# Performance work log

Measured on AMD Instinct MI355X. Metric: run time of the kernel, lower is better.

Reference implementation:

```python
import jax, jax.numpy as jnp
import numpy as np

EPS = 1e-8

def rms_norm(x, scale):
    # norm(2,-1)/sqrt(d); x / (rms + eps) * scale
    d = x.shape[-1]
    norm = jnp.sqrt(jnp.sum(x * x, axis=-1, keepdims=True))
    rms = norm / jnp.sqrt(jnp.asarray(d, x.dtype))
    return scale * (x / (rms + EPS))

def setup_inputs() -> dict:
    key = jax.random.key(0)
    B, N, C, FF = 2, 2048, 1024, 4096
    ks = jax.random.split(key, 12)
    s = 0.02
    return {
        "x":  jax.random.normal(ks[0], (B, N, C), jnp.float32),
        "wq": jax.random.normal(ks[1], (C, C), jnp.float32) * s,
        "bq": jnp.zeros((C,), jnp.float32),
        "wk": jax.random.normal(ks[2], (C, C), jnp.float32) * s,
        "bk": jnp.zeros((C,), jnp.float32),
        "wv": jax.random.normal(ks[3], (C, C), jnp.float32) * s,
        "bv": jnp.zeros((C,), jnp.float32),
        "wo": jax.random.normal(ks[4], (C, C), jnp.float32) * s,
        "bo": jnp.zeros((C,), jnp.float32),
        "scale1": jnp.ones((C,), jnp.float32),
        "scale2": jnp.ones((C,), jnp.float32),
        "w1": jax.random.normal(ks[5], (C, FF), jnp.float32) * s,
        "b1": jnp.zeros((FF,), jnp.float32),
        "w2": jax.random.normal(ks[6], (FF, C), jnp.float32) * s,
        "b2": jnp.zeros((C,), jnp.float32),
    }

def reference(x, wq, bq, wk, bk, wv, bv, wo, bo, scale1, scale2, w1, b1, w2, b2):
    B, N, C = x.shape
    H = 16
    D = C // H

    residual = x
    xn = rms_norm(x, scale1)

    def heads(y):  # [B,N,C] -> [B,H,N,D]
        return y.reshape(B, N, H, D).transpose(0, 2, 1, 3)

    q = heads(xn @ wq + bq)
    k = heads(xn @ wk + bk)
    v = heads(xn @ wv + bv)

    # apply_rotary_pos_emb with cos=sin=1: q' = q - roll(q,1,-1), same for k
    q = q - jnp.roll(q, 1, axis=-1)
    k = k - jnp.roll(k, 1, axis=-1)

    # explicit attention (no causal mask in original)
    scores = jnp.einsum('bhnd,bhmd->bhnm', q, k) / jnp.sqrt(jnp.asarray(D, x.dtype))
    probs = jax.nn.softmax(scores, axis=-1)
    attn = jnp.einsum('bhnm,bhmd->bhnd', probs, v)
    attn = attn.transpose(0, 2, 1, 3).reshape(B, N, C)
    attn = attn @ wo + bo

    x = residual + attn
    residual = x
    xn = rms_norm(x, scale2)
    h = jax.nn.gelu(xn @ w1 + b1, approximate=False)  # torch GELU default = exact
    ffn_out = h @ w2 + b2
    return residual + ffn_out
```

## Files before the change

### kernel.cpp

```cpp
#include <hip/hip_runtime.h>
#include <hip/hip_bf16.h>
#include <math.h>

typedef unsigned short u16;
typedef short s16x8 __attribute__((ext_vector_type(8)));
typedef short s16x4 __attribute__((ext_vector_type(4)));
typedef __bf16 bf16x8v __attribute__((ext_vector_type(8)));
typedef float f32x4 __attribute__((ext_vector_type(4)));
typedef unsigned short u16x4 __attribute__((ext_vector_type(4)));

struct Ptr4 { float* p[4]; };
struct TW6 {
    const float* w[6]; u16* o[6]; int mode[6];
    const float *bq, *bk, *bv; float* bqkv;
};

__device__ __forceinline__ u16 f2b(float f) {
    __hip_bfloat16 h = __float2bfloat16(f);
    return __builtin_bit_cast(u16, h);
}

__device__ __forceinline__ float exp2_fast(float x) {
#if __has_builtin(__builtin_amdgcn_exp2f)
    return __builtin_amdgcn_exp2f(x);
#else
    return exp2f(x);
#endif
}

__device__ __forceinline__ f32x4 mfma16(s16x8 a, s16x8 b, f32x4 c) {
    return __builtin_amdgcn_mfma_f32_16x16x32_bf16(
        __builtin_bit_cast(bf16x8v, a), __builtin_bit_cast(bf16x8v, b), c, 0, 0, 0);
}

__device__ __forceinline__ void gl_lds16(const void* g, void* l) {
    typedef const unsigned int __attribute__((address_space(1))) * gp_t;
    typedef unsigned int __attribute__((address_space(3))) * lp_t;
    __builtin_amdgcn_global_load_lds((gp_t)(unsigned long long)g,
                                     (lp_t)(unsigned int)(unsigned long long)l,
                                     16, 0, 0);
}

__device__ __forceinline__ float gelu_fast(float v) {
    float u = 1.5957691216f * (v + 0.044715f * v * v * v);
    return v / (1.f + __expf(-u));
}

#define QSCALE 0.1803368801111244f

__global__ __launch_bounds__(256) void prep_weights(TW6 io) {
    const int z = blockIdx.z, bx = blockIdx.x, by = blockIdx.y;
    const float* W; u16* Wt; int mode = 0, N_, K_, n0, k0;
    if (z < 4) {
        if (bx >= 32) {
            if (z == 0 && bx < 44 && by == 0) {
                const int i = (bx - 32) * 256 + threadIdx.x;
                const int d = i & 1023;
                const int dp = (d & ~63) | ((d + 63) & 63);
                float v;
                if (i < 1024) v = QSCALE * (io.bq[d] - io.bq[dp]);
                else if (i < 2048) v = io.bk[d] - io.bk[dp];
                else v = io.bv[d];
                io.bqkv[i] = v;
            }
            return;
        }
        W = io.w[z]; Wt = io.o[z]; mode = io.mode[z];
        N_ = 1024; K_ = 1024; n0 = bx * 32; k0 = by * 32;
    } else if (z == 4) {
        W = io.w[4]; Wt = io.o[4]; N_ = 4096; K_ = 1024; n0 = bx * 32; k0 = by * 32;
    } else {
        W = io.w[5]; Wt = io.o[5]; N_ = 1024; K_ = 4096; n0 = by * 32; k0 = bx * 32;
    }
    __shared__ u16 tile[32][33];
    const int tx = threadIdx.x & 31, ty = threadIdx.x >> 5;
    const int n = n0 + tx;
    const int np = (n & ~63) | ((n + 63) & 63);
    const float s = (mode == 1) ? QSCALE : 1.f;
#pragma unroll
    for (int i = 0; i < 32; i += 8) {
        const size_t r = (size_t)(k0 + ty + i) * N_;
        float v = W[r + n];
        if (mode) v = (v - W[r + np]) * s;
        tile[ty + i][tx] = f2b(v);
    }
    __syncthreads();
#pragma unroll
    for (int i = 0; i < 32; i += 8)
        Wt[(size_t)(n0 + ty + i) * K_ + k0 + tx] = tile[tx][ty + i];
}

__global__ __launch_bounds__(256) void transpose_v(const u16* __restrict__ qkv,
                                                   u16* __restrict__ vT) {
    __shared__ u16 tile[32][33];
    const int tx = threadIdx.x & 31, ty = threadIdx.x >> 5;
    const int n0 = blockIdx.x * 32, d0 = blockIdx.y * 32, bh = blockIdx.z;
    const int b = bh >> 4, h = bh & 15;
#pragma unroll
    for (int i = 0; i < 32; i += 8)
        tile[ty + i][tx] =
            qkv[(size_t)(b * 2048 + n0 + ty + i) * 3072 + 2048 + h * 64 + d0 + tx];
    __syncthreads();
#pragma unroll
    for (int i = 0; i < 32; i += 8)
        vT[((size_t)bh * 64 + d0 + ty + i) * 2048 + n0 + tx] = tile[tx][ty + i];
}

__global__ __launch_bounds__(256) void rmsnorm_kernel(const float* __restrict__ x,
                                                      const float* __restrict__ scale,
                                                      u16* __restrict__ out) {
    __shared__ float red[4];
    const int t = threadIdx.x, row = blockIdx.x;
    const float4* xr = (const float4*)(x + (size_t)row * 1024);
    float4 v = xr[t];
    float ss = v.x * v.x + v.y * v.y + v.z * v.z + v.w * v.w;
#pragma unroll
    for (int off = 1; off < 64; off <<= 1) ss += __shfl_xor(ss, off);
    if ((t & 63) == 0) red[t >> 6] = ss;
    __syncthreads();
    float tot = red[0] + red[1] + red[2] + red[3];
    float inv = 1.f / (sqrtf(tot * (1.f / 1024.f)) + 1e-8f);
    const float4* sr = (const float4*)scale;
    float4 s = sr[t];
    u16x4 o;
    o[0] = f2b(v.x * inv * s.x);
    o[1] = f2b(v.y * inv * s.y);
    o[2] = f2b(v.z * inv * s.z);
    o[3] = f2b(v.w * inv * s.w);
    ((u16x4*)(out + (size_t)row * 1024))[t] = o;
}

template <int EPI>
__global__ __launch_bounds__(256) void gemm_kernel(const u16* __restrict__ A,
                                                   const u16* __restrict__ Bt,
                                                   const float* __restrict__ bias,
                                                   const float* __restrict__ resid,
                                                   void* __restrict__ outp,
                                                   int M, int N, int K) {
    __shared__ __align__(16) u16 As[128 * 64];
    __shared__ __align__(16) u16 Bs[128 * 64];
    const int t = threadIdx.x, lane = t & 63;
    const int w = t >> 6, wm = (w >> 1) * 64, wn = (w & 1) * 64;
    const int c = lane & 15, qd = lane >> 4;
    const int n0 = blockIdx.x * 128, m0 = blockIdx.y * 128;

    const int srow = t >> 3;
    const int sch8 = ((t & 7) ^ (srow & 7)) * 8;
    const u16* Ag = A + (size_t)(m0 + srow) * K + sch8;
    const u16* Bg = Bt + (size_t)(n0 + srow) * K + sch8;
    const size_t rstride = (size_t)32 * K;

    f32x4 acc[4][4] = {};
    for (int kt = 0; kt < K; kt += 64) {
        __syncthreads();
#pragma unroll
        for (int g = 0; g < 4; g++) {
            gl_lds16(Ag + g * rstride, &As[t * 8 + g * 2048]);
            gl_lds16(Bg + g * rstride, &Bs[t * 8 + g * 2048]);
        }
        Ag += 64;
        Bg += 64;
        __syncthreads();
#pragma unroll
        for (int s = 0; s < 2; s++) {
            s16x8 a[4], b[4];
#pragma unroll
            for (int im = 0; im < 4; im++)
                a[im] = *(const s16x8*)&As[(wm + im * 16 + c) * 64 +
                                           (((s * 4 + qd) ^ (c & 7)) * 8)];
#pragma unroll
            for (int jn = 0; jn < 4; jn++)
                b[jn] = *(const s16x8*)&Bs[(wn + jn * 16 + c) * 64 +
                                           (((s * 4 + qd) ^ (c & 7)) * 8)];
#pragma unroll
            for (int im = 0; im < 4; im++)
#pragma unroll
                for (int jn = 0; jn < 4; jn++)
                    acc[im][jn] = mfma16(a[im], b[jn], acc[im][jn]);
        }
    }

#pragma unroll
    for (int im = 0; im < 4; im++) {
#pragma unroll
        for (int jn = 0; jn < 4; jn++) {
            const int colg = n0 + wn + jn * 16 + c;
            const float bv = bias[colg];
#pragma unroll
            for (int r = 0; r < 4; r++) {
                const int rowg = m0 + wm + im * 16 + qd * 4 + r;
                const size_t off = (size_t)rowg * N + colg;
                float v = acc[im][jn][r] + bv;
                if (EPI == 0) {
                    ((u16*)outp)[off] = f2b(v);
                } else if (EPI == 1) {
                    ((float*)outp)[off] = v + resid[off];
                } else {
                    ((u16*)outp)[off] = f2b(gelu_fast(v));
                }
            }
        }
    }
}

__global__ __launch_bounds__(512, 2) void gemm256_gelu(const u16* __restrict__ A,
                                                       const u16* __restrict__ Bt,
                                                       const float* __restrict__ bias,
                                                       u16* __restrict__ outp) {
    __shared__ __align__(16) u16 sm[65536];
    u16* As = sm;
    u16* Bs = sm + 32768;

    const int t = threadIdx.x, lane = t & 63, w = t >> 6;
    const int c = lane & 15, qd = lane >> 4;
    const int wm = (w >> 2) * 128, wn = (w & 3) * 64;

    const int id = (int)blockIdx.x;
    const int l = (id & 7) * 32 + (id >> 3);
    const int m0 = (l >> 4) * 256, n0 = (l & 15) * 256;

    const int srow = t >> 3;
    const int sch8 = ((t & 7) ^ (srow & 7)) * 8;
    const u16* Ag = A + (size_t)(m0 + srow) * 1024 + sch8;
    const u16* Bg = Bt + (size_t)(n0 + srow) * 1024 + sch8;

    float bv[4];
#pragma unroll
    for (int n = 0; n < 4; ++n) bv[n] = bias[n0 + wn + n * 16 + c];
    asm volatile("" ::: "memory");

    auto stageA = [&](int kt, int h, int s) {
        const u16* src = Ag + (size_t)(h * 128) * 1024 + kt * 64;
        u16* dst = As + s * 16384 + h * 8192 + t * 8;
        gl_lds16(src, dst);
        gl_lds16(src + (size_t)64 * 1024, dst + 4096);
    };
    auto stageB = [&](int kt, int h, int s) {
        const u16* src = Bg + (size_t)(h * 128) * 1024 + kt * 64;
        u16* dst = Bs + s * 16384 + h * 8192 + t * 8;
        gl_lds16(src, dst);
        gl_lds16(src + (size_t)64 * 1024, dst + 4096);
    };

    stageA(0, 0, 0); stageA(0, 1, 0);
    stageB(0, 0, 0); stageB(0, 1, 0);
    stageB(1, 0, 1); stageB(1, 1, 1);
    asm volatile("s_waitcnt vmcnt(4)" ::: "memory");
    __builtin_amdgcn_s_barrier();
    __builtin_amdgcn_sched_barrier(0);

    f32x4 acc[8][4] = {};

    for (int it = 0; it < 8; ++it) {
        const int ktA = 2 * it, ktB = 2 * it + 1;
        s16x8 bf[4][2];

#pragma unroll
        for (int q = 0; q < 4; ++q) {
            s16x8 af[2][2];
            if (q == 0) {
#pragma unroll
                for (int n = 0; n < 4; ++n)
#pragma unroll
                    for (int ks = 0; ks < 2; ++ks)
                        bf[n][ks] = *(const s16x8*)&Bs[(wn + n * 16 + c) * 64 +
                                                       (((ks * 4 + qd) ^ (c & 7)) * 8)];
            }
#pragma unroll
            for (int mm = 0; mm < 2; ++mm)
#pragma unroll
                for (int ks = 0; ks < 2; ++ks)
                    af[mm][ks] = *(const s16x8*)&As[(wm + (2 * q + mm) * 16 + c) * 64 +
                                                    (((ks * 4 + qd) ^ (c & 7)) * 8)];
            if (q == 0) {
                stageA(ktB, 0, 1);
            } else if (q == 1) {
                stageA(ktB, 1, 1);
                if (ktA + 2 < 16) stageB(ktA + 2, 0, 0);
            } else if (q == 2) {
                if (ktA + 2 < 16) stageB(ktA + 2, 1, 0);
            }
            __builtin_amdgcn_s_barrier();
            asm volatile("s_waitcnt lgkmcnt(0)" ::: "memory");
            __builtin_amdgcn_sched_barrier(0);
            __builtin_amdgcn_s_setprio(1);
#pragma unroll
            for (int mm = 0; mm < 2; ++mm)
#pragma unroll
                for (int n = 0; n < 4; ++n)
#pragma unroll
                    for (int ks = 0; ks < 2; ++ks)
                        acc[2 * q + mm][n] =
                            mfma16(af[mm][ks], bf[n][ks], acc[2 * q + mm][n]);
            __builtin_amdgcn_s_setprio(0);
            if (q == 3) {
                if (it < 7)
                    asm volatile("s_waitcnt vmcnt(4)" ::: "memory");
                else
                    asm volatile("s_waitcnt vmcnt(0)" ::: "memory");
            }
            __builtin_amdgcn_s_barrier();
        }

#pragma unroll
        for (int q = 0; q < 4; ++q) {
            s16x8 af[2][2];
            if (q == 0) {
#pragma unroll
                for (int n = 0; n < 4; ++n)
#pragma unroll
                    for (int ks = 0; ks < 2; ++ks)
                        bf[n][ks] = *(const s16x8*)&Bs[16384 + (wn + n * 16 + c) * 64 +
                                                       (((ks * 4 + qd) ^ (c & 7)) * 8)];
            }
#pragma unroll
            for (int mm = 0; mm < 2; ++mm)
#pragma unroll
                for (int ks = 0; ks < 2; ++ks)
                    af[mm][ks] = *(const s16x8*)&As[16384 + (wm + (2 * q + mm) * 16 + c) * 64 +
                                                    (((ks * 4 + qd) ^ (c & 7)) * 8)];
            if (q == 0) {
                if (ktA + 2 < 16) stageA(ktA + 2, 0, 0);
            } else if (q == 1) {
                if (ktA + 2 < 16) stageA(ktA + 2, 1, 0);
            } else if (q == 2) {
                if (ktB + 2 < 16) stageB(ktB + 2, 0, 1);
            } else {
                if (ktB + 2 < 16) stageB(ktB + 2, 1, 1);
            }
            __builtin_amdgcn_s_barrier();
            asm volatile("s_waitcnt lgkmcnt(0)" ::: "memory");
            __builtin_amdgcn_sched_barrier(0);
            __builtin_amdgcn_s_setprio(1);
#pragma unroll
            for (int mm = 0; mm < 2; ++mm)
#pragma unroll
                for (int n = 0; n < 4; ++n)
#pragma unroll
                    for (int ks = 0; ks < 2; ++ks)
                        acc[2 * q + mm][n] =
                            mfma16(af[mm][ks], bf[n][ks], acc[2 * q + mm][n]);
            __builtin_amdgcn_s_setprio(0);
            if (q == 3 && it < 7)
                asm volatile("s_waitcnt vmcnt(4)" ::: "memory");
            __builtin_amdgcn_s_barrier();
        }
    }

#pragma unroll
    for (int m = 0; m < 8; ++m)
#pragma unroll
        for (int n = 0; n < 4; ++n) {
            const int colg = n0 + wn + n * 16 + c;
#pragma unroll
            for (int r = 0; r < 4; ++r) {
                const int rowg = m0 + wm + m * 16 + qd * 4 + r;
                outp[(size_t)rowg * 4096 + colg] =
                    f2b(gelu_fast(acc[m][n][r] + bv[n]));
            }
        }
}

__global__ __launch_bounds__(256) void gemm_splitk(const u16* __restrict__ A,
                                                   const u16* __restrict__ Bt,
                                                   Ptr4 parts,
                                                   int N, int Ktot, int Kc) {
    __shared__ __align__(16) u16 As[128 * 64];
    __shared__ __align__(16) u16 Bs[128 * 64];
    const int t = threadIdx.x, lane = t & 63;
    const int w = t >> 6, wm = (w >> 1) * 64, wn = (w & 1) * 64;
    const int c = lane & 15, qd = lane >> 4;
    const int n0 = blockIdx.x * 128, m0 = blockIdx.y * 128;
    const int z = blockIdx.z;
    float* out = parts.p[z];

    const int srow = t >> 3;
    const int sch8 = ((t & 7) ^ (srow & 7)) * 8;
    const u16* Ag = A + (size_t)(m0 + srow) * Ktot + z * Kc + sch8;
    const u16* Bg = Bt + (size_t)(n0 + srow) * Ktot + z * Kc + sch8;
    const size_t rstride = (size_t)32 * Ktot;

    f32x4 acc[4][4] = {};
    for (int kt = 0; kt < Kc; kt += 64) {
        __syncthreads();
#pragma unroll
        for (int g = 0; g < 4; g++) {
            gl_lds16(Ag + g * rstride, &As[t * 8 + g * 2048]);
            gl_lds16(Bg + g * rstride, &Bs[t * 8 + g * 2048]);
        }
        Ag += 64;
        Bg += 64;
        __syncthreads();
#pragma unroll
        for (int s = 0; s < 2; s++) {
            s16x8 a[4], b[4];
#pragma unroll
            for (int im = 0; im < 4; im++)
                a[im] = *(const s16x8*)&As[(wm + im * 16 + c) * 64 +
                                           (((s * 4 + qd) ^ (c & 7)) * 8)];
#pragma unroll
            for (int jn = 0; jn < 4; jn++)
                b[jn] = *(const s16x8*)&Bs[(wn + jn * 16 + c) * 64 +
                                           (((s * 4 + qd) ^ (c & 7)) * 8)];
#pragma unroll
            for (int im = 0; im < 4; im++)
#pragma unroll
                for (int jn = 0; jn < 4; jn++)
                    acc[im][jn] = mfma16(a[im], b[jn], acc[im][jn]);
        }
    }

#pragma unroll
    for (int im = 0; im < 4; im++)
#pragma unroll
        for (int jn = 0; jn < 4; jn++) {
            const int colg = n0 + wn + jn * 16 + c;
#pragma unroll
            for (int r = 0; r < 4; r++) {
                const int rowg = m0 + wm + im * 16 + qd * 4 + r;
                out[(size_t)rowg * N + colg] = acc[im][jn][r];
            }
        }
}

template <int S, bool NORM>
__global__ __launch_bounds__(256) void reduce_kernel(Ptr4 parts,
                                                     const float* __restrict__ bias,
                                                     const float* __restrict__ resid,
                                                     const float* __restrict__ scale,
                                                     float* __restrict__ yout,
                                                     u16* __restrict__ xnout) {
    __shared__ float red[4];
    const int t = threadIdx.x, row = blockIdx.x;
    const size_t base = (size_t)row * 1024;
    float4 v = ((const float4*)(resid + base))[t];
    float4 bv = ((const float4*)bias)[t];
    v.x += bv.x; v.y += bv.y; v.z += bv.z; v.w += bv.w;
#pragma unroll
    for (int s = 0; s < S; s++) {
        float4 pv = ((const float4*)(parts.p[s] + base))[t];
        v.x += pv.x; v.y += pv.y; v.z += pv.z; v.w += pv.w;
    }
    ((float4*)(yout + base))[t] = v;
    if (NORM) {
        float ss = v.x * v.x + v.y * v.y + v.z * v.z + v.w * v.w;
#pragma unroll
        for (int off = 1; off < 64; off <<= 1) ss += __shfl_xor(ss, off);
        if ((t & 63) == 0) red[t >> 6] = ss;
        __syncthreads();
        float tot = red[0] + red[1] + red[2] + red[3];
        float inv = 1.f / (sqrtf(tot * (1.f / 1024.f)) + 1e-8f);
        float4 s = ((const float4*)scale)[t];
        u16x4 o;
        o[0] = f2b(v.x * inv * s.x);
        o[1] = f2b(v.y * inv * s.y);
        o[2] = f2b(v.z * inv * s.z);
        o[3] = f2b(v.w * inv * s.w);
        ((u16x4*)(xnout + base))[t] = o;
    }
}

__global__ __launch_bounds__(256, 2) void attn_kernel(const u16* __restrict__ qkv,
                                                      const u16* __restrict__ vT,
                                                      u16* __restrict__ attn) {
    __shared__ __align__(16) char smem[65536];
    __shared__ float LS[4][64];
    u16* SM = (u16*)smem;

    const int t = threadIdx.x, lane = t & 63, w = t >> 6;
    const int c = lane & 15, g = lane >> 4;

    const int id = blockIdx.x;
    const int logical = (id & 7) * 128 + (id >> 3);
    const int bh = logical >> 5, qb = logical & 31;
    const int b = bh >> 4, h = bh & 15;
    const int q0 = qb * 64;
    const size_t rowbase = (size_t)b * 2048;

    const u16* kg = qkv + rowbase * 3072 + 1024 + h * 64;
    const u16* vg = vT + (size_t)bh * 64 * 2048;

    u16* WS = SM + w * 8192;

    const int kr = lane >> 3, ks8 = lane & 7;
    const int ksw = (ks8 ^ (kr & 7)) * 8;
    const int vr = lane >> 1, vh = (lane & 1) * 8;

    auto stage = [&](int it, int bi) {
        u16* B = WS + bi * 2048;
        const u16* kq = kg + (size_t)(it * 64 + w * 16) * 3072;
        const u16* vq = vg + it * 64 + w * 16;
        gl_lds16(kq + (size_t)kr * 3072 + ksw,       &B[lane * 8]);
        gl_lds16(kq + (size_t)(kr + 8) * 3072 + ksw, &B[512 + lane * 8]);
        gl_lds16(vq + (size_t)vr * 2048 + vh,        &B[1024 + lane * 8]);
        gl_lds16(vq + (size_t)(vr + 32) * 2048 + vh, &B[1536 + lane * 8]);
    };

    s16x8 qf[4][2];
    {
        const u16* qg = qkv + (rowbase + q0) * 3072 + h * 64;
#pragma unroll
        for (int jn = 0; jn < 4; jn++)
#pragma unroll
            for (int ks = 0; ks < 2; ks++)
                qf[jn][ks] = *(const s16x8*)&qg[(size_t)(jn * 16 + c) * 3072 +
                                                ks * 32 + g * 8];
    }

    stage(0, 0);
    stage(1, 1);
    stage(2, 2);
    stage(3, 3);

    f32x4 acc[4][4] = {};
    float ls[4] = {};

    for (int j = 0; j < 16; j++) {
        if (j < 15)
            asm volatile("s_waitcnt vmcnt(8)" ::: "memory");
        else
            asm volatile("s_waitcnt vmcnt(0)" ::: "memory");
        __builtin_amdgcn_sched_barrier(0);

        const u16* Kb0 = WS + ((2 * j) & 3) * 2048;
        const u16* Kb1 = WS + ((2 * j + 1) & 3) * 2048;
        const u16* Vb0 = Kb0 + 1024;
        const u16* Vb1 = Kb1 + 1024;

        s16x8 kf0[2], kf1[2];
#pragma unroll
        for (int ks = 0; ks < 2; ks++) {
            const int sw = ((ks * 4 + g) ^ (c & 7)) * 8;
            kf0[ks] = *(const s16x8*)&Kb0[c * 64 + sw];
            kf1[ks] = *(const s16x8*)&Kb1[c * 64 + sw];
        }
        s16x8 vf[4];
#pragma unroll
        for (int im = 0; im < 4; im++) {
            s16x4 v0 = *(const s16x4*)&Vb0[(im * 16 + c) * 16 + g * 4];
            s16x4 v1 = *(const s16x4*)&Vb1[(im * 16 + c) * 16 + g * 4];
            vf[im] = __builtin_shufflevector(v0, v1, 0, 1, 2, 3, 4, 5, 6, 7);
        }

        s16x8 pb[4];
        {
            f32x4 sc[4] = {};
            __builtin_amdgcn_s_setprio(1);
#pragma unroll
            for (int ks = 0; ks < 2; ks++)
#pragma unroll
                for (int jn = 0; jn < 4; jn++)
                    sc[jn] = mfma16(kf0[ks], qf[jn][ks], sc[jn]);
            __builtin_amdgcn_s_setprio(0);
#pragma unroll
            for (int jn = 0; jn < 4; jn++) {
                float p0 = exp2_fast(sc[jn][0]);
                float p1 = exp2_fast(sc[jn][1]);
                float p2 = exp2_fast(sc[jn][2]);
                float p3 = exp2_fast(sc[jn][3]);
                ls[jn] += (p0 + p1) + (p2 + p3);
                pb[jn][0] = f2b(p0); pb[jn][1] = f2b(p1);
                pb[jn][2] = f2b(p2); pb[jn][3] = f2b(p3);
            }
        }
        {
            f32x4 sc[4] = {};
            __builtin_amdgcn_s_setprio(1);
#pragma unroll
            for (int ks = 0; ks < 2; ks++)
#pragma unroll
                for (int jn = 0; jn < 4; jn++)
                    sc[jn] = mfma16(kf1[ks], qf[jn][ks], sc[jn]);
            __builtin_amdgcn_s_setprio(0);
#pragma unroll
            for (int jn = 0; jn < 4; jn++) {
                float p0 = exp2_fast(sc[jn][0]);
                float p1 = exp2_fast(sc[jn][1]);
                float p2 = exp2_fast(sc[jn][2]);
                float p3 = exp2_fast(sc[jn][3]);
                ls[jn] += (p0 + p1) + (p2 + p3);
                pb[jn][4] = f2b(p0); pb[jn][5] = f2b(p1);
                pb[jn][6] = f2b(p2); pb[jn][7] = f2b(p3);
            }
        }

        __builtin_amdgcn_s_setprio(1);
#pragma unroll
        for (int im = 0; im < 4; im++)
#pragma unroll
            for (int jn = 0; jn < 4; jn++)
                acc[im][jn] = mfma16(vf[im], pb[jn], acc[im][jn]);
        __builtin_amdgcn_s_setprio(0);

        __builtin_amdgcn_sched_barrier(0);
        if (j < 14) {
            stage(2 * j + 4, (2 * j) & 3);
            stage(2 * j + 5, (2 * j + 1) & 3);
        }
    }

#pragma unroll
    for (int jn = 0; jn < 4; jn++) {
        float v = ls[jn];
        v += __shfl_xor(v, 16);
        v += __shfl_xor(v, 32);
        ls[jn] = v;
    }
    if (lane < 16) {
#pragma unroll
        for (int jn = 0; jn < 4; jn++) LS[w][jn * 16 + lane] = ls[jn];
    }

    float* SC = (float*)smem;
#pragma unroll
    for (int src = 3; src >= 1; --src) {
        __syncthreads();
        if (w == src) {
#pragma unroll
            for (int im = 0; im < 4; im++)
#pragma unroll
                for (int jn = 0; jn < 4; jn++)
#pragma unroll
                    for (int r = 0; r < 4; r++)
                        SC[(im * 16 + g * 4 + r) * 66 + jn * 16 + c] =
                            acc[im][jn][r];
        }
        __syncthreads();
        if (w == src - 1) {
#pragma unroll
            for (int im = 0; im < 4; im++)
#pragma unroll
                for (int jn = 0; jn < 4; jn++)
#pragma unroll
                    for (int r = 0; r < 4; r++)
                        acc[im][jn][r] +=
                            SC[(im * 16 + g * 4 + r) * 66 + jn * 16 + c];
        }
    }
    __syncthreads();

    u16* OT = (u16*)smem;
    if (w == 0) {
#pragma unroll
        for (int jn = 0; jn < 4; jn++) {
            const int q = jn * 16 + c;
            const float inv = 1.f / (LS[0][q] + LS[1][q] + LS[2][q] + LS[3][q]);
#pragma unroll
            for (int im = 0; im < 4; im++)
#pragma unroll
                for (int r = 0; r < 4; r++)
                    OT[q * 72 + im * 16 + g * 4 + r] = f2b(acc[im][jn][r] * inv);
        }
    }
    __syncthreads();

    {
        const int q = t >> 2, d0 = (t & 3) * 16;
        const int grow = b * 2048 + q0 + q;
        u16* dst = attn + (size_t)grow * 1024 + h * 64 + d0;
        *(s16x8*)dst = *(const s16x8*)&OT[q * 72 + d0];
        *((s16x8*)dst + 1) = *((const s16x8*)&OT[q * 72 + d0] + 1);
    }
}

extern "C" void kernel_launch(void* const* d_in, const int* in_sizes, int n_in,
                              void* d_out, int out_size, void* d_ws, size_t ws_size,
                              hipStream_t stream) {
    const float* x = (const float*)d_in[0];
    const float* wq = (const float*)d_in[1];
    const float* bq = (const float*)d_in[2];
    const float* wk = (const float*)d_in[3];
    const float* bk = (const float*)d_in[4];
    const float* wv = (const float*)d_in[5];
    const float* bv = (const float*)d_in[6];
    const float* wo = (const float*)d_in[7];
    const float* bo = (const float*)d_in[8];
    const float* scale1 = (const float*)d_in[9];
    const float* scale2 = (const float*)d_in[10];
    const float* w1 = (const float*)d_in[11];
    const float* b1 = (const float*)d_in[12];
    const float* w2 = (const float*)d_in[13];
    const float* b2 = (const float*)d_in[14];
    float* out = (float*)d_out;

    char* ws = (char*)d_ws;
    size_t off = 0;
    auto alloc = [&](size_t bytes) -> char* {
        char* p = ws + off;
        off += (bytes + 255) & ~(size_t)255;
        return p;
    };
    u16* wqkvT = (u16*)alloc((size_t)3072 * 1024 * 2);
    u16* woT   = (u16*)alloc((size_t)1024 * 1024 * 2);
    u16* w1T   = (u16*)alloc((size_t)4096 * 1024 * 2);
    u16* w2T   = (u16*)alloc((size_t)1024 * 4096 * 2);
    float* bqkv = (float*)alloc(3072 * 4);
    u16* xn    = (u16*)alloc((size_t)4096 * 1024 * 2);
    u16* qkv   = (u16*)alloc((size_t)4096 * 3072 * 2);
    u16* vT    = (u16*)alloc((size_t)32 * 64 * 2048 * 2);
    u16* attnb = (u16*)alloc((size_t)4096 * 1024 * 2);
    float* y1  = (float*)alloc((size_t)4096 * 1024 * 4);
    u16* hbuf  = (u16*)alloc((size_t)4096 * 4096 * 2);

    const size_t SPLIT = (size_t)4096 * 1024;
    Ptr4 po; po.p[0] = (float*)qkv; po.p[1] = (float*)qkv + SPLIT;
    po.p[2] = nullptr; po.p[3] = nullptr;
    Ptr4 pf; pf.p[0] = (float*)xn; pf.p[1] = (float*)xn + SPLIT;
    pf.p[2] = (float*)xn + 2 * SPLIT; pf.p[3] = (float*)wqkvT;

    dim3 blk(256);

    TW6 tw;
    tw.w[0] = wq; tw.o[0] = wqkvT;                          tw.mode[0] = 1;
    tw.w[1] = wk; tw.o[1] = wqkvT + (size_t)1024 * 1024;    tw.mode[1] = 2;
    tw.w[2] = wv; tw.o[2] = wqkvT + (size_t)2048 * 1024;    tw.mode[2] = 0;
    tw.w[3] = wo; tw.o[3] = woT;                            tw.mode[3] = 0;
    tw.w[4] = w1; tw.o[4] = w1T;                            tw.mode[4] = 0;
    tw.w[5] = w2; tw.o[5] = w2T;                            tw.mode[5] = 0;
    tw.bq = bq; tw.bk = bk; tw.bv = bv; tw.bqkv = bqkv;
    prep_weights<<<dim3(128, 32, 6), blk, 0, stream>>>(tw);

    rmsnorm_kernel<<<4096, blk, 0, stream>>>(x, scale1, xn);
    gemm_kernel<0><<<dim3(24, 32), blk, 0, stream>>>(xn, wqkvT, bqkv, nullptr, qkv, 4096, 3072, 1024);
    transpose_v<<<dim3(64, 2, 32), blk, 0, stream>>>(qkv, vT);
    attn_kernel<<<dim3(1024), blk, 0, stream>>>(qkv, vT, attnb);
    gemm_splitk<<<dim3(8, 32, 2), blk, 0, stream>>>(attnb, woT, po, 1024, 1024, 512);
    reduce_kernel<2, true><<<4096, blk, 0, stream>>>(po, bo, x, scale2, y1, xn);
    gemm256_gelu<<<dim3(256), dim3(512), 0, stream>>>(xn, w1T, b1, hbuf);
    gemm_splitk<<<dim3(8, 32, 4), blk, 0, stream>>>(hbuf, w2T, pf, 1024, 4096, 1024);
    reduce_kernel<4, false><<<4096, blk, 0, stream>>>(pf, b2, y1, nullptr, out, nullptr);
}
```

Measured before the change: 356.8 us.

## Generalize 256x256 pipelined GEMM and use it for QKV and split-K FFN2

```diff
diff --git a/kernel.cpp b/kernel.cpp
--- a/kernel.cpp
+++ b/kernel.cpp
@@ -131,82 +131,13 @@
 }
 
 template <int EPI>
-__global__ __launch_bounds__(256) void gemm_kernel(const u16* __restrict__ A,
-                                                   const u16* __restrict__ Bt,
-                                                   const float* __restrict__ bias,
-                                                   const float* __restrict__ resid,
-                                                   void* __restrict__ outp,
-                                                   int M, int N, int K) {
-    __shared__ __align__(16) u16 As[128 * 64];
-    __shared__ __align__(16) u16 Bs[128 * 64];
-    const int t = threadIdx.x, lane = t & 63;
-    const int w = t >> 6, wm = (w >> 1) * 64, wn = (w & 1) * 64;
-    const int c = lane & 15, qd = lane >> 4;
-    const int n0 = blockIdx.x * 128, m0 = blockIdx.y * 128;
-
-    const int srow = t >> 3;
-    const int sch8 = ((t & 7) ^ (srow & 7)) * 8;
-    const u16* Ag = A + (size_t)(m0 + srow) * K + sch8;
-    const u16* Bg = Bt + (size_t)(n0 + srow) * K + sch8;
-    const size_t rstride = (size_t)32 * K;
-
-    f32x4 acc[4][4] = {};
-    for (int kt = 0; kt < K; kt += 64) {
-        __syncthreads();
-#pragma unroll
-        for (int g = 0; g < 4; g++) {
-            gl_lds16(Ag + g * rstride, &As[t * 8 + g * 2048]);
-            gl_lds16(Bg + g * rstride, &Bs[t * 8 + g * 2048]);
-        }
-        Ag += 64;
-        Bg += 64;
-        __syncthreads();
-#pragma unroll
-        for (int s = 0; s < 2; s++) {
-            s16x8 a[4], b[4];
-#pragma unroll
-            for (int im = 0; im < 4; im++)
-                a[im] = *(const s16x8*)&As[(wm + im * 16 + c) * 64 +
-                                           (((s * 4 + qd) ^ (c & 7)) * 8)];
-#pragma unroll
-            for (int jn = 0; jn < 4; jn++)
-                b[jn] = *(const s16x8*)&Bs[(wn + jn * 16 + c) * 64 +
-                                           (((s * 4 + qd) ^ (c & 7)) * 8)];
-#pragma unroll
-            for (int im = 0; im < 4; im++)
-#pragma unroll
-                for (int jn = 0; jn < 4; jn++)
-                    acc[im][jn] = mfma16(a[im], b[jn], acc[im][jn]);
-        }
-    }
-
-#pragma unroll
-    for (int im = 0; im < 4; im++) {
-#pragma unroll
-        for (int jn = 0; jn < 4; jn++) {
-            const int colg = n0 + wn + jn * 16 + c;
-            const float bv = bias[colg];
-#pragma unroll
-            for (int r = 0; r < 4; r++) {
-                const int rowg = m0 + wm + im * 16 + qd * 4 + r;
-                const size_t off = (size_t)rowg * N + colg;
-                float v = acc[im][jn][r] + bv;
-                if (EPI == 0) {
-                    ((u16*)outp)[off] = f2b(v);
-                } else if (EPI == 1) {
-                    ((float*)outp)[off] = v + resid[off];
-                } else {
-                    ((u16*)outp)[off] = f2b(gelu_fast(v));
-                }
-            }
-        }
-    }
-}
-
-__global__ __launch_bounds__(512, 2) void gemm256_gelu(const u16* __restrict__ A,
-                                                       const u16* __restrict__ Bt,
-                                                       const float* __restrict__ bias,
-                                                       u16* __restrict__ outp) {
+__global__ __launch_bounds__(512, 2) void gemm256(const u16* __restrict__ A,
+                                                  const u16* __restrict__ Bt,
+                                                  const float* __restrict__ bias,
+                                                  Ptr4 parts,
+                                                  u16* __restrict__ outp,
+                                                  int Nout, int nTN, int cpx,
+                                                  int Ktot) {
     __shared__ __align__(16) u16 sm[65536];
     u16* As = sm;
     u16* Bs = sm + 32768;
@@ -216,30 +147,34 @@
     const int wm = (w >> 2) * 128, wn = (w & 3) * 64;
 
     const int id = (int)blockIdx.x;
-    const int l = (id & 7) * 32 + (id >> 3);
-    const int m0 = (l >> 4) * 256, n0 = (l & 15) * 256;
+    const int l = (id & 7) * cpx + (id >> 3);
+    const int m0 = (l / nTN) * 256, n0 = (l % nTN) * 256;
+    const int k0 = (EPI == 3) ? (int)blockIdx.y * 1024 : 0;
+    float* pout = (EPI == 3) ? parts.p[blockIdx.y] : nullptr;
 
     const int srow = t >> 3;
     const int sch8 = ((t & 7) ^ (srow & 7)) * 8;
-    const u16* Ag = A + (size_t)(m0 + srow) * 1024 + sch8;
-    const u16* Bg = Bt + (size_t)(n0 + srow) * 1024 + sch8;
+    const u16* Ag = A + (size_t)(m0 + srow) * Ktot + k0 + sch8;
+    const u16* Bg = Bt + (size_t)(n0 + srow) * Ktot + k0 + sch8;
 
     float bv[4];
-#pragma unroll
-    for (int n = 0; n < 4; ++n) bv[n] = bias[n0 + wn + n * 16 + c];
-    asm volatile("" ::: "memory");
+    if (EPI != 3) {
+#pragma unroll
+        for (int n = 0; n < 4; ++n) bv[n] = bias[n0 + wn + n * 16 + c];
+        asm volatile("" ::: "memory");
+    }
 
     auto stageA = [&](int kt, int h, int s) {
-        const u16* src = Ag + (size_t)(h * 128) * 1024 + kt * 64;
+        const u16* src = Ag + (size_t)(h * 128) * Ktot + kt * 64;
         u16* dst = As + s * 16384 + h * 8192 + t * 8;
         gl_lds16(src, dst);
-        gl_lds16(src + (size_t)64 * 1024, dst + 4096);
+        gl_lds16(src + (size_t)64 * Ktot, dst + 4096);
     };
     auto stageB = [&](int kt, int h, int s) {
-        const u16* src = Bg + (size_t)(h * 128) * 1024 + kt * 64;
+        const u16* src = Bg + (size_t)(h * 128) * Ktot + kt * 64;
         u16* dst = Bs + s * 16384 + h * 8192 + t * 8;
         gl_lds16(src, dst);
-        gl_lds16(src + (size_t)64 * 1024, dst + 4096);
+        gl_lds16(src + (size_t)64 * Ktot, dst + 4096);
     };
 
     stageA(0, 0, 0); stageA(0, 1, 0);
@@ -355,8 +290,14 @@
 #pragma unroll
             for (int r = 0; r < 4; ++r) {
                 const int rowg = m0 + wm + m * 16 + qd * 4 + r;
-                outp[(size_t)rowg * 4096 + colg] =
-                    f2b(gelu_fast(acc[m][n][r] + bv[n]));
+                if (EPI == 0) {
+                    outp[(size_t)rowg * Nout + colg] = f2b(acc[m][n][r] + bv[n]);
+                } else if (EPI == 2) {
+                    outp[(size_t)rowg * Nout + colg] =
+                        f2b(gelu_fast(acc[m][n][r] + bv[n]));
+                } else {
+                    pout[(size_t)rowg * 1024 + colg] = acc[m][n][r];
+                }
             }
         }
 }
@@ -707,6 +648,7 @@
     po.p[2] = nullptr; po.p[3] = nullptr;
     Ptr4 pf; pf.p[0] = (float*)xn; pf.p[1] = (float*)xn + SPLIT;
     pf.p[2] = (float*)xn + 2 * SPLIT; pf.p[3] = (float*)wqkvT;
+    Ptr4 pz = {};
 
     dim3 blk(256);
 
@@ -721,12 +663,12 @@
     prep_weights<<<dim3(128, 32, 6), blk, 0, stream>>>(tw);
 
     rmsnorm_kernel<<<4096, blk, 0, stream>>>(x, scale1, xn);
-    gemm_kernel<0><<<dim3(24, 32), blk, 0, stream>>>(xn, wqkvT, bqkv, nullptr, qkv, 4096, 3072, 1024);
+    gemm256<0><<<dim3(192), dim3(512), 0, stream>>>(xn, wqkvT, bqkv, pz, qkv, 3072, 12, 24, 1024);
     transpose_v<<<dim3(64, 2, 32), blk, 0, stream>>>(qkv, vT);
     attn_kernel<<<dim3(1024), blk, 0, stream>>>(qkv, vT, attnb);
     gemm_splitk<<<dim3(8, 32, 2), blk, 0, stream>>>(attnb, woT, po, 1024, 1024, 512);
     reduce_kernel<2, true><<<4096, blk, 0, stream>>>(po, bo, x, scale2, y1, xn);
-    gemm256_gelu<<<dim3(256), dim3(512), 0, stream>>>(xn, w1T, b1, hbuf);
-    gemm_splitk<<<dim3(8, 32, 4), blk, 0, stream>>>(hbuf, w2T, pf, 1024, 4096, 1024);
+    gemm256<2><<<dim3(256), dim3(512), 0, stream>>>(xn, w1T, b1, pz, hbuf, 4096, 16, 32, 1024);
+    gemm256<3><<<dim3(64, 4), dim3(512), 0, stream>>>(hbuf, w2T, nullptr, pf, nullptr, 1024, 4, 8, 4096);
     reduce_kernel<4, false><<<4096, blk, 0, stream>>>(pf, b2, y1, nullptr, out, nullptr);
 }
```

Measured after the change: 341.9 us. -4.2%, faster.
